# Kernel optimization log

Measured on AMD Instinct MI355X. Metric: run time of the kernel, lower is better.

The kernel has to match this reference:

```python
import jax, jax.numpy as jnp
import numpy as np

B, S, D_IN, D_OUT = 8, 2048, 768, 768

def setup_inputs() -> dict:
    key = jax.random.key(0)
    k1, k2 = jax.random.split(key)
    x = jax.random.normal(k1, (B, S, D_IN), dtype=jnp.float32)
    QKV = jax.random.normal(k2, (3, D_IN, D_OUT), dtype=jnp.float32) * 0.02
    return {"x": x, "QKV": QKV}

def reference(x, QKV):
    # Single-head self-attention; scale uses sqrt(d_in) as in the original.
    q = jnp.einsum('bsd,de->bse', x, QKV[0])  # [B,S,D_OUT]
    k = jnp.einsum('bsd,de->bse', x, QKV[1])
    v = jnp.einsum('bsd,de->bse', x, QKV[2])
    scale = 1.0 / jnp.sqrt(jnp.asarray(x.shape[-1], dtype=x.dtype))
    scores = jnp.einsum('bqe,bke->bqk', q, k) * scale  # [B,S,S]
    probs = jax.nn.softmax(scores, axis=-1)
    return jnp.einsum('bqk,bke->bqe', probs, v)  # [B,S,D_OUT]
```

## Files before the change

### kernel.cpp

```cpp
#include <hip/hip_runtime.h>
#include <hip/hip_bf16.h>
#include <cstdint>


#define NB 8
#define NS 2048
#define ND 768
#define NQK 1536
#define MTOT 16384

using f32x4 = __attribute__((ext_vector_type(4))) float;
using s16x8 = __attribute__((ext_vector_type(8))) short;

struct alignas(16) bf16x8 { __hip_bfloat16 h[8]; };
struct alignas(8)  bf16x4 { __hip_bfloat16 h[4]; };

#define CVT_BLOCKS 4096
#define WT_BLOCKS 1728
__global__ __launch_bounds__(256) void preprocess_kernel(const float* __restrict__ x,
                                                         __hip_bfloat16* __restrict__ xb,
                                                         const float* __restrict__ W,
                                                         __hip_bfloat16* __restrict__ Wt,
                                                         float* __restrict__ rowsum) {
    __shared__ float tile[32][33];
    const int tid = threadIdx.x;
    if (blockIdx.x < CVT_BLOCKS) {
#pragma unroll
        for (int it = 0; it < 3; ++it) {
            const int i = (it * CVT_BLOCKS + blockIdx.x) * 256 + tid;
            const f32x4 v = __builtin_nontemporal_load((const f32x4*)x + i);
            bf16x4 o;
            o.h[0] = __float2bfloat16(v[0]);
            o.h[1] = __float2bfloat16(v[1]);
            o.h[2] = __float2bfloat16(v[2]);
            o.h[3] = __float2bfloat16(v[3]);
            ((bf16x4*)xb)[i] = o;
        }
    } else if (blockIdx.x < CVT_BLOCKS + WT_BLOCKS) {
        const int bid = blockIdx.x - CVT_BLOCKS;
        const int e = bid / 576, rem = bid % 576;
        const int k0 = (rem / 24) * 32, n0 = (rem % 24) * 32;
        const float* Wp = W + (size_t)e * ND * ND;
        __hip_bfloat16* Wo = Wt + (size_t)e * ND * ND;
        {
            const int ty = tid >> 3, tx = tid & 7;
            const f32x4 v = __builtin_nontemporal_load(
                (const f32x4*)&Wp[(k0 + ty) * ND + n0 + tx * 4]);
#pragma unroll
            for (int q = 0; q < 4; ++q) tile[ty][tx * 4 + q] = v[q];
        }
        __syncthreads();
        {
            const int np = tid >> 3, kq = tid & 7;
            bf16x4 o;
#pragma unroll
            for (int q = 0; q < 4; ++q) o.h[q] = __float2bfloat16(tile[kq * 4 + q][np]);
            *(bf16x4*)&Wo[(long)(n0 + np) * ND + k0 + kq * 4] = o;
        }
    } else {
        const int i = (blockIdx.x - CVT_BLOCKS - WT_BLOCKS) * 1024 + tid * 4;
        f32x4 z = {0.f, 0.f, 0.f, 0.f};
        *(f32x4*)(rowsum + i) = z;
    }
}

__device__ __forceinline__ void storeC(float* p, float v) { *p = v; }
__device__ __forceinline__ void storeC(__hip_bfloat16* p, float v) { *p = __float2bfloat16(v); }

typedef const __attribute__((address_space(1))) void* gp;
typedef __attribute__((address_space(3))) void* sp;

#define SBAR() asm volatile("s_barrier" ::: "memory")

#define STAGE_AH(H_, T_) do {                                                              \
    char* d_ = smem + (((T_) & 1) * 65536) + (H_) * 16384 + ldsOff;                        \
    __builtin_amdgcn_global_load_lds((gp)(gA + (long)((H_) * 128) * lda + (T_) * 64),      \
                                     (sp)d_, 16, 0, 0);                                    \
    __builtin_amdgcn_global_load_lds((gp)(gA + (long)((H_) * 128 + 64) * lda + (T_) * 64), \
                                     (sp)(d_ + 8192), 16, 0, 0);                           \
} while (0)

#define STAGE_BH(H_, T_) do {                                                              \
    char* d_ = smem + (((T_) & 1) * 65536) + 32768 + (H_) * 16384 + ldsOff;                \
    __builtin_amdgcn_global_load_lds((gp)(gB + (long)((H_) * 128) * ldb + (T_) * 64),      \
                                     (sp)d_, 16, 0, 0);                                    \
    __builtin_amdgcn_global_load_lds((gp)(gB + (long)((H_) * 128 + 64) * ldb + (T_) * 64), \
                                     (sp)(d_ + 8192), 16, 0, 0);                           \
} while (0)

#define MFMA_Q(MI0_, NI0_) do {                                                            \
    _Pragma("unroll") for (int m_ = 0; m_ < 4; ++m_)                                       \
    _Pragma("unroll") for (int n_ = 0; n_ < 2; ++n_)                                       \
    _Pragma("unroll") for (int k_ = 0; k_ < 2; ++k_)                                       \
        acc[(MI0_) + m_][(NI0_) + n_] = __builtin_amdgcn_mfma_f32_16x16x32_bf16(           \
            af[m_][k_], bf[(NI0_) + n_][k_], acc[(MI0_) + m_][(NI0_) + n_], 0, 0, 0);      \
} while (0)

#define KTILE(T_, SP1_, SP3_, SP4_, VM_) do {                                              \
    char* abase = smem + (((T_) & 1) * 65536);                                             \
    char* bbase = abase + 32768;                                                           \
                  \
    _Pragma("unroll") for (int m_ = 0; m_ < 4; ++m_) {                                     \
        af[m_][0] = *(const s16x8*)(abase + aoff + m_ * 2048 + ck0);                       \
        af[m_][1] = *(const s16x8*)(abase + aoff + m_ * 2048 + ck1);                       \
    }                                                                                      \
    _Pragma("unroll") for (int n_ = 0; n_ < 2; ++n_) {                                     \
        bf[n_][0] = *(const s16x8*)(bbase + boff + n_ * 2048 + ck0);                       \
        bf[n_][1] = *(const s16x8*)(bbase + boff + n_ * 2048 + ck1);                       \
    }                                                                                      \
    if (SP1_) STAGE_AH(1, (T_) + 1);                                                       \
    asm volatile("s_waitcnt lgkmcnt(8)" ::: "memory");                                     \
    SBAR();                                                                                \
    asm volatile("s_waitcnt lgkmcnt(0)" ::: "memory");                                     \
    __builtin_amdgcn_sched_barrier(0);                                                     \
    __builtin_amdgcn_s_setprio(1);                                                         \
    MFMA_Q(0, 0);                                                                          \
    __builtin_amdgcn_s_setprio(0);                                                         \
    SBAR();                                                                                \
           \
    _Pragma("unroll") for (int n_ = 0; n_ < 2; ++n_) {                                     \
        bf[2 + n_][0] = *(const s16x8*)(bbase + boff + (2 + n_) * 2048 + ck0);             \
        bf[2 + n_][1] = *(const s16x8*)(bbase + boff + (2 + n_) * 2048 + ck1);             \
    }                                                                                      \
    SBAR();                                                                                \
    asm volatile("s_waitcnt lgkmcnt(0)" ::: "memory");                                     \
    __builtin_amdgcn_sched_barrier(0);                                                     \
    __builtin_amdgcn_s_setprio(1);                                                         \
    MFMA_Q(0, 2);                                                                          \
    __builtin_amdgcn_s_setprio(0);                                                         \
    SBAR();                                                                                \
           \
    _Pragma("unroll") for (int m_ = 0; m_ < 4; ++m_) {                                     \
        af[m_][0] = *(const s16x8*)(abase + aoff + (4 + m_) * 2048 + ck0);                 \
        af[m_][1] = *(const s16x8*)(abase + aoff + (4 + m_) * 2048 + ck1);                 \
    }                                                                                      \
    if (SP3_) STAGE_BH(0, (T_) + 2);                                                       \
    SBAR();                                                                                \
    asm volatile("s_waitcnt lgkmcnt(0)" ::: "memory");                                     \
    __builtin_amdgcn_sched_barrier(0);                                                     \
    __builtin_amdgcn_s_setprio(1);                                                         \
    MFMA_Q(4, 2);                                                                          \
    __builtin_amdgcn_s_setprio(0);                                                         \
    SBAR();                                                                                \
            \
    if (SP4_) { STAGE_AH(0, (T_) + 2); STAGE_BH(1, (T_) + 2); }                            \
    if ((VM_) == 0) { asm volatile("s_waitcnt vmcnt(6)" ::: "memory"); }                   \
    else if ((VM_) == 1) { asm volatile("s_waitcnt vmcnt(0)" ::: "memory"); }              \
    SBAR();                                                                                \
    __builtin_amdgcn_s_setprio(1);                                                         \
    MFMA_Q(4, 0);                                                                          \
    __builtin_amdgcn_s_setprio(0);                                                         \
    SBAR();                                                                                \
} while (0)

template <typename OutT, int EPI, int NKT, bool BATCH_X>
__global__ __launch_bounds__(512, 2) void gemm256_kernel(
    const __hip_bfloat16* __restrict__ A,
    const __hip_bfloat16* __restrict__ Bm,
    OutT* __restrict__ C,
    __hip_bfloat16* __restrict__ vtOut,
    float* __restrict__ rowsum,
    int lda, int ldb, int ldc,
    long sA, long sB, long sC, float scale) {
    static_assert(NKT >= 3, "pipeline needs >= 3 K-tiles");
    __shared__ alignas(16) char smem[131072];

    int b, tileM, tileN;
    if (BATCH_X) {
        b = blockIdx.x; tileN = blockIdx.y * 256; tileM = blockIdx.z * 256;
    } else {
        b = 0;
        const int l0 = blockIdx.y * gridDim.x + blockIdx.x;
        const int cpx = (gridDim.x * gridDim.y) >> 3;
        const int tl = (l0 & 7) * cpx + (l0 >> 3);
        tileN = (tl % gridDim.x) * 256;
        tileM = (tl / gridDim.x) * 256;
    }
    A  += (long)b * sA;
    Bm += (long)b * sB;
    C  += (long)b * sC;

    const int tid  = threadIdx.x;
    const int lane = tid & 63;
    const int wid  = tid >> 6;
    const int wr   = wid >> 2;
    const int wc   = wid & 3;
    const int quad = lane >> 4;
    const int lrow = lane & 15;

    const int srow = tid >> 3;
    const int scol = ((tid & 7) ^ (srow & 7)) << 3;
    const __hip_bfloat16* gA = A + (long)(tileM + srow) * lda + scol;
    const __hip_bfloat16* gB = Bm + (long)(tileN + srow) * ldb + scol;
    const int ldsOff = tid * 16;

    const int swa  = lrow & 7;
    const int ck0  = (quad ^ swa) << 4;
    const int ck1  = ((quad + 4) ^ swa) << 4;
    const int aoff = wr * 16384 + lrow * 128;
    const int boff = wc * 8192 + lrow * 128;

    f32x4 acc[8][4];
    const f32x4 zero = {0.f, 0.f, 0.f, 0.f};
#pragma unroll
    for (int i = 0; i < 8; ++i)
#pragma unroll
        for (int j = 0; j < 4; ++j) acc[i][j] = zero;

    STAGE_AH(0, 0); STAGE_BH(0, 0); STAGE_BH(1, 0); STAGE_AH(1, 0);
    asm volatile("s_waitcnt vmcnt(4)" ::: "memory");
    STAGE_AH(0, 1); STAGE_BH(0, 1); STAGE_BH(1, 1);
    asm volatile("s_waitcnt vmcnt(6)" ::: "memory");
    SBAR();

    s16x8 af[4][2], bf[4][2];
#pragma unroll 1
    for (int t = 0; t < NKT - 2; ++t) { KTILE(t, 1, 1, 1, 0); }
    KTILE(NKT - 2, 1, 0, 0, 1);
    KTILE(NKT - 1, 0, 0, 0, 2);

    if (EPI == 2 && tileN >= NQK) {
        char* T = smem;
#pragma unroll
        for (int mi = 0; mi < 8; ++mi) {
#pragma unroll
            for (int ni = 0; ni < 4; ++ni) {
                const int d = wc * 64 + ni * 16 + lrow;
                const int s = wr * 128 + mi * 16 + quad * 4;
                bf16x4 g;
#pragma unroll
                for (int r = 0; r < 4; ++r) g.h[r] = __float2bfloat16(acc[mi][ni][r]);
                const int off = d * 512 + ((((s >> 3) ^ (d & 31)) << 4) | ((s & 4) << 1));
                *(bf16x4*)(T + off) = g;
            }
        }
        __syncthreads();
        const int dl = tid >> 1, half = tid & 1;
        const long bb = tileM >> 11;
        const int s0 = tileM & (NS - 1);
        const long dg = (long)(tileN - NQK) + dl;
        __hip_bfloat16* dst = vtOut + (bb * ND + dg) * NS + s0;
#pragma unroll
        for (int cc = 0; cc < 16; ++cc) {
            const int c2 = half * 16 + cc;
            s16x8 val = *(const s16x8*)(T + dl * 512 + ((c2 ^ (dl & 31)) << 4));
            *(s16x8*)(dst + c2 * 8) = val;
        }
        return;
    }

    if (EPI == 3) {
#pragma unroll
        for (int mi = 0; mi < 8; ++mi) {
            float rs[4] = {0.f, 0.f, 0.f, 0.f};
#pragma unroll
            for (int ni = 0; ni < 4; ++ni) {
                const int col = tileN + wc * 64 + ni * 16 + lrow;
#pragma unroll
                for (int r = 0; r < 4; ++r) {
                    const int row = tileM + wr * 128 + mi * 16 + quad * 4 + r;
                    const float e = __expf(acc[mi][ni][r] * scale);
                    const __hip_bfloat16 h = __float2bfloat16(e);
                    storeC(C + (long)row * ldc + col, __bfloat162float(h));
                    rs[r] += __bfloat162float(h);
                }
            }
#pragma unroll
            for (int r = 0; r < 4; ++r) {
#pragma unroll
                for (int off = 1; off < 16; off <<= 1) rs[r] += __shfl_xor(rs[r], off);
            }
            if (lrow == 0) {
#pragma unroll
                for (int r = 0; r < 4; ++r)
                    atomicAdd(rowsum + (long)b * NS + tileM + wr * 128 + mi * 16 + quad * 4 + r,
                              rs[r]);
            }
        }
        return;
    }

    if (EPI == 4) {
#pragma unroll
        for (int mi = 0; mi < 8; ++mi) {
            float inv[4];
#pragma unroll
            for (int r = 0; r < 4; ++r)
                inv[r] = 1.0f / rowsum[(long)b * NS + tileM + wr * 128 + mi * 16 + quad * 4 + r];
#pragma unroll
            for (int ni = 0; ni < 4; ++ni) {
                const int col = tileN + wc * 64 + ni * 16 + lrow;
#pragma unroll
                for (int r = 0; r < 4; ++r) {
                    const int row = tileM + wr * 128 + mi * 16 + quad * 4 + r;
                    storeC(C + (long)row * ldc + col, acc[mi][ni][r] * inv[r]);
                }
            }
        }
        return;
    }

#pragma unroll
    for (int mi = 0; mi < 8; ++mi) {
#pragma unroll
        for (int ni = 0; ni < 4; ++ni) {
            const int col = tileN + wc * 64 + ni * 16 + lrow;
#pragma unroll
            for (int r = 0; r < 4; ++r) {
                const int row = tileM + wr * 128 + mi * 16 + quad * 4 + r;
                storeC(C + (long)row * ldc + col, acc[mi][ni][r] * scale);
            }
        }
    }
}

extern "C" void kernel_launch(void* const* d_in, const int* in_sizes, int n_in,
                              void* d_out, int out_size, void* d_ws, size_t ws_size,
                              hipStream_t stream) {
    const float* x   = (const float*)d_in[0];
    const float* QKV = (const float*)d_in[1];
    float* out = (float*)d_out;

    uint8_t* ws = (uint8_t*)d_ws;
    constexpr size_t XB_BYTES  = (size_t)MTOT * ND * 2;
    constexpr size_t WT_BYTES  = (size_t)3 * ND * ND * 2;
    constexpr size_t QKV_BYTES = (size_t)MTOT * NQK * 2;
    constexpr size_t VT_BYTES  = (size_t)NB * ND * NS * 2;
    constexpr size_t PR_BYTES  = (size_t)MTOT * NS * 2;
    __hip_bfloat16* xb    = (__hip_bfloat16*)(ws);
    __hip_bfloat16* Wt    = (__hip_bfloat16*)(ws + XB_BYTES);
    __hip_bfloat16* qkvb  = (__hip_bfloat16*)(ws + XB_BYTES + WT_BYTES);
    __hip_bfloat16* vt    = (__hip_bfloat16*)(ws + XB_BYTES + WT_BYTES + QKV_BYTES);
    __hip_bfloat16* probs = (__hip_bfloat16*)(ws + XB_BYTES + WT_BYTES + QKV_BYTES + VT_BYTES);
    float*          rowsum= (float*)(ws + XB_BYTES + WT_BYTES + QKV_BYTES + VT_BYTES + PR_BYTES);

    const float scale = 0.03608439182435161f;

    preprocess_kernel<<<CVT_BLOCKS + WT_BLOCKS + 16, 256, 0, stream>>>(x, xb, QKV, Wt, rowsum);
    gemm256_kernel<__hip_bfloat16, 2, 12, false><<<dim3(2304 / 256, MTOT / 256, 1), 512, 0, stream>>>(
        xb, Wt, qkvb, vt, nullptr, ND, ND, NQK, 0, 0, 0, 1.0f);
    gemm256_kernel<__hip_bfloat16, 3, 12, true><<<dim3(NB, NS / 256, NS / 256), 512, 0, stream>>>(
        qkvb, qkvb + ND, probs, nullptr, rowsum, NQK, NQK, NS,
        (long)NS * NQK, (long)NS * NQK, (long)NS * NS, scale);
    gemm256_kernel<float, 4, 32, true><<<dim3(NB, ND / 256, NS / 256), 512, 0, stream>>>(
        probs, vt, out, nullptr, rowsum, NS, NS, ND,
        (long)NS * NS, (long)ND * NS, (long)NS * ND, 1.0f);
}
```

Baseline: 295.3 us.

## Remap warp subtiles across LDS halves and restructure K-tile prefetch schedule

Each warp's 128x64 output tile is now split into quadrants that straddle both 128-row halves of the A and B LDS tiles, instead of lying in one contiguous half. The epilogue index maps (V-transpose, exp/rowsum, normalize, scale) are rewritten to match. With both A halves consumed partway through, every global-to-LDS stage for tile T+2 can be issued inside KTILE T with a single SP flag. The prologue now fully stages two tiles, and vmcnt waits are adjusted to match. The aim is a more uniform prefetch schedule that hides global load latency better, at the cost of requiring at least 4 K-tiles and adding some risk in the wait counts.

Measured after the change: 302.8 us. 2.5% more time.

```diff
diff --git a/kernel.cpp b/kernel.cpp
--- a/kernel.cpp
+++ b/kernel.cpp
@@ -96,10 +96,10 @@
             af[m_][k_], bf[(NI0_) + n_][k_], acc[(MI0_) + m_][(NI0_) + n_], 0, 0, 0);      \
 } while (0)
 
-#define KTILE(T_, SP1_, SP3_, SP4_, VM_) do {                                              \
+#define KTILE(T_, SP_, VM_) do {                                                           \
     char* abase = smem + (((T_) & 1) * 65536);                                             \
     char* bbase = abase + 32768;                                                           \
-                  \
+                        \
     _Pragma("unroll") for (int m_ = 0; m_ < 4; ++m_) {                                     \
         af[m_][0] = *(const s16x8*)(abase + aoff + m_ * 2048 + ck0);                       \
         af[m_][1] = *(const s16x8*)(abase + aoff + m_ * 2048 + ck1);                       \
@@ -108,7 +108,6 @@
         bf[n_][0] = *(const s16x8*)(bbase + boff + n_ * 2048 + ck0);                       \
         bf[n_][1] = *(const s16x8*)(bbase + boff + n_ * 2048 + ck1);                       \
     }                                                                                      \
-    if (SP1_) STAGE_AH(1, (T_) + 1);                                                       \
     asm volatile("s_waitcnt lgkmcnt(8)" ::: "memory");                                     \
     SBAR();                                                                                \
     asm volatile("s_waitcnt lgkmcnt(0)" ::: "memory");                                     \
@@ -117,11 +116,12 @@
     MFMA_Q(0, 0);                                                                          \
     __builtin_amdgcn_s_setprio(0);                                                         \
     SBAR();                                                                                \
-           \
+                \
     _Pragma("unroll") for (int n_ = 0; n_ < 2; ++n_) {                                     \
-        bf[2 + n_][0] = *(const s16x8*)(bbase + boff + (2 + n_) * 2048 + ck0);             \
-        bf[2 + n_][1] = *(const s16x8*)(bbase + boff + (2 + n_) * 2048 + ck1);             \
+        bf[2 + n_][0] = *(const s16x8*)(bbase + 16384 + boff + n_ * 2048 + ck0);           \
+        bf[2 + n_][1] = *(const s16x8*)(bbase + 16384 + boff + n_ * 2048 + ck1);           \
     }                                                                                      \
+    if (SP_) STAGE_AH(0, (T_) + 2);                                                        \
     SBAR();                                                                                \
     asm volatile("s_waitcnt lgkmcnt(0)" ::: "memory");                                     \
     __builtin_amdgcn_sched_barrier(0);                                                     \
@@ -129,12 +129,12 @@
     MFMA_Q(0, 2);                                                                          \
     __builtin_amdgcn_s_setprio(0);                                                         \
     SBAR();                                                                                \
-           \
+                      \
     _Pragma("unroll") for (int m_ = 0; m_ < 4; ++m_) {                                     \
-        af[m_][0] = *(const s16x8*)(abase + aoff + (4 + m_) * 2048 + ck0);                 \
-        af[m_][1] = *(const s16x8*)(abase + aoff + (4 + m_) * 2048 + ck1);                 \
+        af[m_][0] = *(const s16x8*)(abase + 16384 + aoff + m_ * 2048 + ck0);               \
+        af[m_][1] = *(const s16x8*)(abase + 16384 + aoff + m_ * 2048 + ck1);               \
     }                                                                                      \
-    if (SP3_) STAGE_BH(0, (T_) + 2);                                                       \
+    if (SP_) STAGE_BH(0, (T_) + 2);                                                       \
     SBAR();                                                                                \
     asm volatile("s_waitcnt lgkmcnt(0)" ::: "memory");                                     \
     __builtin_amdgcn_sched_barrier(0);                                                     \
@@ -142,9 +142,9 @@
     MFMA_Q(4, 2);                                                                          \
     __builtin_amdgcn_s_setprio(0);                                                         \
     SBAR();                                                                                \
-            \
-    if (SP4_) { STAGE_AH(0, (T_) + 2); STAGE_BH(1, (T_) + 2); }                            \
-    if ((VM_) == 0) { asm volatile("s_waitcnt vmcnt(6)" ::: "memory"); }                   \
+          \
+    if (SP_) { STAGE_BH(1, (T_) + 2); STAGE_AH(1, (T_) + 2); }                             \
+    if ((VM_) == 0) { asm volatile("s_waitcnt vmcnt(8)" ::: "memory"); }                   \
     else if ((VM_) == 1) { asm volatile("s_waitcnt vmcnt(0)" ::: "memory"); }              \
     SBAR();                                                                                \
     __builtin_amdgcn_s_setprio(1);                                                         \
@@ -162,7 +162,7 @@
     float* __restrict__ rowsum,
     int lda, int ldb, int ldc,
     long sA, long sB, long sC, float scale) {
-    static_assert(NKT >= 3, "pipeline needs >= 3 K-tiles");
+    static_assert(NKT >= 4, "pipeline needs >= 4 K-tiles");
     __shared__ alignas(16) char smem[131072];
 
     int b, tileM, tileN;
@@ -197,8 +197,8 @@
     const int swa  = lrow & 7;
     const int ck0  = (quad ^ swa) << 4;
     const int ck1  = ((quad + 4) ^ swa) << 4;
-    const int aoff = wr * 16384 + lrow * 128;
-    const int boff = wc * 8192 + lrow * 128;
+    const int aoff = wr * 8192 + lrow * 128;
+    const int boff = wc * 4096 + lrow * 128;
 
     f32x4 acc[8][4];
     const f32x4 zero = {0.f, 0.f, 0.f, 0.f};
@@ -208,16 +208,15 @@
         for (int j = 0; j < 4; ++j) acc[i][j] = zero;
 
     STAGE_AH(0, 0); STAGE_BH(0, 0); STAGE_BH(1, 0); STAGE_AH(1, 0);
-    asm volatile("s_waitcnt vmcnt(4)" ::: "memory");
-    STAGE_AH(0, 1); STAGE_BH(0, 1); STAGE_BH(1, 1);
-    asm volatile("s_waitcnt vmcnt(6)" ::: "memory");
+    STAGE_AH(0, 1); STAGE_BH(0, 1); STAGE_BH(1, 1); STAGE_AH(1, 1);
+    asm volatile("s_waitcnt vmcnt(8)" ::: "memory");
     SBAR();
 
     s16x8 af[4][2], bf[4][2];
 #pragma unroll 1
-    for (int t = 0; t < NKT - 2; ++t) { KTILE(t, 1, 1, 1, 0); }
-    KTILE(NKT - 2, 1, 0, 0, 1);
-    KTILE(NKT - 1, 0, 0, 0, 2);
+    for (int t = 0; t <= NKT - 3; ++t) { KTILE(t, 1, 0); }
+    KTILE(NKT - 2, 0, 1);
+    KTILE(NKT - 1, 0, 2);
 
     if (EPI == 2 && tileN >= NQK) {
         char* T = smem;
@@ -225,8 +224,8 @@
         for (int mi = 0; mi < 8; ++mi) {
 #pragma unroll
             for (int ni = 0; ni < 4; ++ni) {
-                const int d = wc * 64 + ni * 16 + lrow;
-                const int s = wr * 128 + mi * 16 + quad * 4;
+                const int d = ((ni >> 1) << 7) + wc * 32 + ((ni & 1) << 4) + lrow;
+                const int s = ((mi >> 2) << 7) + wr * 64 + ((mi & 3) << 4) + quad * 4;
                 bf16x4 g;
 #pragma unroll
                 for (int r = 0; r < 4; ++r) g.h[r] = __float2bfloat16(acc[mi][ni][r]);
@@ -252,16 +251,16 @@
     if (EPI == 3) {
 #pragma unroll
         for (int mi = 0; mi < 8; ++mi) {
+            const int rowb = tileM + ((mi >> 2) << 7) + wr * 64 + ((mi & 3) << 4) + quad * 4;
             float rs[4] = {0.f, 0.f, 0.f, 0.f};
 #pragma unroll
             for (int ni = 0; ni < 4; ++ni) {
-                const int col = tileN + wc * 64 + ni * 16 + lrow;
+                const int col = tileN + ((ni >> 1) << 7) + wc * 32 + ((ni & 1) << 4) + lrow;
 #pragma unroll
                 for (int r = 0; r < 4; ++r) {
-                    const int row = tileM + wr * 128 + mi * 16 + quad * 4 + r;
                     const float e = __expf(acc[mi][ni][r] * scale);
                     const __hip_bfloat16 h = __float2bfloat16(e);
-                    storeC(C + (long)row * ldc + col, __bfloat162float(h));
+                    storeC(C + (long)(rowb + r) * ldc + col, __bfloat162float(h));
                     rs[r] += __bfloat162float(h);
                 }
             }
@@ -273,8 +272,7 @@
             if (lrow == 0) {
 #pragma unroll
                 for (int r = 0; r < 4; ++r)
-                    atomicAdd(rowsum + (long)b * NS + tileM + wr * 128 + mi * 16 + quad * 4 + r,
-                              rs[r]);
+                    atomicAdd(rowsum + (long)b * NS + rowb + r, rs[r]);
             }
         }
         return;
@@ -283,18 +281,17 @@
     if (EPI == 4) {
 #pragma unroll
         for (int mi = 0; mi < 8; ++mi) {
+            const int rowb = tileM + ((mi >> 2) << 7) + wr * 64 + ((mi & 3) << 4) + quad * 4;
             float inv[4];
 #pragma unroll
             for (int r = 0; r < 4; ++r)
-                inv[r] = 1.0f / rowsum[(long)b * NS + tileM + wr * 128 + mi * 16 + quad * 4 + r];
+                inv[r] = 1.0f / rowsum[(long)b * NS + rowb + r];
 #pragma unroll
             for (int ni = 0; ni < 4; ++ni) {
-                const int col = tileN + wc * 64 + ni * 16 + lrow;
-#pragma unroll
-                for (int r = 0; r < 4; ++r) {
-                    const int row = tileM + wr * 128 + mi * 16 + quad * 4 + r;
-                    storeC(C + (long)row * ldc + col, acc[mi][ni][r] * inv[r]);
-                }
+                const int col = tileN + ((ni >> 1) << 7) + wc * 32 + ((ni & 1) << 4) + lrow;
+#pragma unroll
+                for (int r = 0; r < 4; ++r)
+                    storeC(C + (long)(rowb + r) * ldc + col, acc[mi][ni][r] * inv[r]);
             }
         }
         return;
@@ -302,14 +299,13 @@
 
 #pragma unroll
     for (int mi = 0; mi < 8; ++mi) {
+        const int rowb = tileM + ((mi >> 2) << 7) + wr * 64 + ((mi & 3) << 4) + quad * 4;
 #pragma unroll
         for (int ni = 0; ni < 4; ++ni) {
-            const int col = tileN + wc * 64 + ni * 16 + lrow;
-#pragma unroll
-            for (int r = 0; r < 4; ++r) {
-                const int row = tileM + wr * 128 + mi * 16 + quad * 4 + r;
-                storeC(C + (long)row * ldc + col, acc[mi][ni][r] * scale);
-            }
+            const int col = tileN + ((ni >> 1) << 7) + wc * 32 + ((ni & 1) << 4) + lrow;
+#pragma unroll
+            for (int r = 0; r < 4; ++r)
+                storeC(C + (long)(rowb + r) * ldc + col, acc[mi][ni][r] * scale);
         }
     }
 }
```
